# Optimization experiments

Measured on AMD Instinct MI355X. Metric: run time of the kernel, lower is better.

Reference implementation:

```python
import jax, jax.numpy as jnp
import numpy as np

EPS = 1e-5

def _conv3x3(x, w, b):
    # standard 3x3 conv, stride 1, padding 1, NCHW/OIHW
    y = jax.lax.conv_general_dilated(x, w, window_strides=(1, 1), padding=((1, 1), (1, 1)),
                                     dimension_numbers=('NCHW', 'OIHW', 'NCHW'))
    return y + b[None, :, None, None]

def _deform_sample(x, offset):
    # x: [B,C,H,W], offset: [B,2*9,H,W] (per kernel point: (dy,dx), torchvision layout)
    # returns bilinear-sampled im2col columns [B,C,9,H,W] with zero padding outside
    B, C, H, W = x.shape
    off = offset.reshape(B, 9, 2, H, W)
    off_y, off_x = off[:, :, 0], off[:, :, 1]                      # [B,9,H,W]
    k = jnp.arange(9)
    ky = (k // 3 - 1).astype(x.dtype)                               # kernel dy in {-1,0,1}
    kx = (k % 3 - 1).astype(x.dtype)                                # kernel dx in {-1,0,1}
    py = jnp.arange(H, dtype=x.dtype)[None, None, :, None] + ky[None, :, None, None] + off_y
    px = jnp.arange(W, dtype=x.dtype)[None, None, None, :] + kx[None, :, None, None] + off_x
    y0 = jnp.floor(py)
    x0 = jnp.floor(px)
    xf = x.reshape(B, C, H * W)
    acc = jnp.zeros((B, C, 9, H, W), x.dtype)
    for dy in (0.0, 1.0):
        for dx in (0.0, 1.0):
            iy = y0 + dy
            ix = x0 + dx
            wgt = (1.0 - jnp.abs(py - iy)) * (1.0 - jnp.abs(px - ix))
            valid = (iy >= 0) & (iy <= H - 1) & (ix >= 0) & (ix <= W - 1)
            wgt = jnp.where(valid, wgt, 0.0)
            idx = jnp.clip(iy, 0, H - 1).astype(jnp.int32) * W + jnp.clip(ix, 0, W - 1).astype(jnp.int32)
            g = jax.vmap(lambda xb, ib: jnp.take(xb, ib, axis=1))(xf, idx.reshape(B, -1))
            acc = acc + wgt[:, None] * g.reshape(B, C, 9, H, W)
    return acc

def setup_inputs() -> dict:
    key = jax.random.key(0)
    ks = jax.random.split(key, 9)
    B, C, O, H, W = 8, 64, 64, 160, 160
    x = jax.random.normal(ks[0], (B, C, H, W), jnp.float32)
    w_off = jax.random.normal(ks[1], (18, C, 3, 3), jnp.float32) * 0.01
    b_off = jax.random.normal(ks[2], (18,), jnp.float32) * 0.01
    w_dcn = jax.random.normal(ks[3], (O, C, 3, 3), jnp.float32) / np.sqrt(C * 9)
    b_dcn = jax.random.normal(ks[4], (O,), jnp.float32) * 0.01
    gamma = 1.0 + 0.1 * jax.random.normal(ks[5], (O,), jnp.float32)
    beta = 0.1 * jax.random.normal(ks[6], (O,), jnp.float32)
    run_mean = 0.1 * jax.random.normal(ks[7], (O,), jnp.float32)
    run_var = 0.5 + jax.random.uniform(ks[8], (O,), jnp.float32)
    return {"x": x, "w_off": w_off, "b_off": b_off, "w_dcn": w_dcn, "b_dcn": b_dcn,
            "gamma": gamma, "beta": beta, "run_mean": run_mean, "run_var": run_var}

def reference(x, w_off, b_off, w_dcn, b_dcn, gamma, beta, run_mean, run_var):
    offset = _conv3x3(x, w_off, b_off)                  # [B,18,H,W]
    cols = _deform_sample(x, offset)                    # [B,C,9,H,W]
    O = w_dcn.shape[0]
    z = jnp.einsum('bckhw,ock->bohw', cols, w_dcn.reshape(O, -1, 9)) + b_dcn[None, :, None, None]
    inv = gamma / jnp.sqrt(run_var + EPS)               # eval-mode BatchNorm
    y = z * inv[None, :, None, None] + (beta - run_mean * inv)[None, :, None, None]
    return jax.nn.relu(y)
```

## Files before the change

kernel.cpp:

```cpp
#include <hip/hip_runtime.h>

#define Hh 160
#define Ww 160
#define HW 25600
#define Bb 8
#define Cc 64
#define Oo 64
#define NPIX (Bb * HW)

#define TROWS 8
#define TCOLS 36
#define TPIX (TROWS * TCOLS)

typedef __bf16 bf16x8 __attribute__((ext_vector_type(8)));
typedef float  f32x4  __attribute__((ext_vector_type(4)));
typedef float  f32x2  __attribute__((ext_vector_type(2)));

__device__ inline unsigned rnd_bf(float a) {
    unsigned u = __float_as_uint(a);
    return (u + 0x7FFFu + ((u >> 16) & 1u)) >> 16;
}
__device__ inline unsigned pack_bf2(float a, float b) {
    unsigned ua = __float_as_uint(a) + 0x8000u;
    unsigned ub = __float_as_uint(b) + 0x8000u;
    return __builtin_amdgcn_perm(ub, ua, 0x07060302);
}
__device__ inline f32x2 up2(unsigned u) {
    f32x2 r;
    r.x = __uint_as_float(u << 16);
    r.y = __uint_as_float(u & 0xffff0000u);
    return r;
}
__device__ inline unsigned blend4(unsigned u00, unsigned u01, unsigned u10, unsigned u11,
                                  float w00, float w01, float w10, float w11) {
    f32x2 r = up2(u00) * w00 + up2(u01) * w01 + up2(u10) * w10 + up2(u11) * w11;
    return pack_bf2(r.x, r.y);
}
union UV { uint4 u; bf16x8 v; };
__device__ inline bf16x8 as_bf(uint4 u) { UV c; c.u = u; return c.v; }

__global__ __launch_bounds__(256) void prep_kernel(
    const float* __restrict__ w_dcn, const float* __restrict__ b_dcn,
    const float* __restrict__ w_off,
    const float* __restrict__ gamma, const float* __restrict__ beta,
    const float* __restrict__ run_mean, const float* __restrict__ run_var,
    unsigned short* __restrict__ wtbf, unsigned short* __restrict__ wofbf,
    float* __restrict__ scaleb)
{
    int i = blockIdx.x * 256 + threadIdx.x;
    if (i < 9 * 8 * 64 * 8) {
        int j = i & 7, l = (i >> 3) & 63, f = (i >> 9) & 7, k = i >> 12;
        int o  = ((f >> 1) << 4) | (l & 15);
        int cc = ((l >> 4) << 3) + ((f & 1) << 5) + j;
        wtbf[i] = (unsigned short)rnd_bf(w_dcn[(o * Cc + cc) * 9 + k]);
    }
    if (i < 9 * 4 * 64 * 8) {
        int j = i & 7, l = (i >> 3) & 63, f = (i >> 9) & 3, k = i >> 11;
        int o  = ((f >> 1) << 4) | (l & 15);
        int cc = ((l >> 4) << 3) + ((f & 1) << 5) + j;
        float v = (o < 18) ? w_off[(o * Cc + cc) * 9 + k] : 0.0f;
        wofbf[i] = (unsigned short)rnd_bf(v);
    }
    if (i < Oo) {
        float inv = gamma[i] * rsqrtf(run_var[i] + 1e-5f);
        scaleb[i]      = inv;
        scaleb[Oo + i] = b_dcn[i] * inv + (beta[i] - run_mean[i] * inv);
    }
}

__global__ __launch_bounds__(256, 4) void xpose_kernel(
    const float* __restrict__ x, unsigned short* __restrict__ xhwc)
{
    __shared__ float tile[64 * 65];
    int blk = blockIdx.x;
    int nb  = (blk & 7) * 400 + (blk >> 3);
    int b = nb / 400, hw0 = (nb % 400) * 64;
    int t = threadIdx.x;
    int lane = t & 63, grp = t >> 6;

    const float* xp = x + (size_t)b * Cc * HW + hw0 + lane;
#pragma unroll
    for (int i = 0; i < 16; ++i) {
        int c = i * 4 + grp;
        tile[lane * 65 + c] = xp[(size_t)c * HW];
    }
    __syncthreads();

    int px  = t >> 2;
    int ch0 = (t & 3) * 16;
    const float* row = tile + px * 65 + ch0;
    unsigned u[8];
#pragma unroll
    for (int j = 0; j < 8; ++j) u[j] = pack_bf2(row[2 * j], row[2 * j + 1]);
    unsigned short* dst = xhwc + ((size_t)(b * HW + hw0 + px)) * 64 + ch0;
    *(uint4*)dst       = make_uint4(u[0], u[1], u[2], u[3]);
    *(uint4*)(dst + 8) = make_uint4(u[4], u[5], u[6], u[7]);
}

#define TRD(PIX, LO, HI) do {                                                  \
    int _pp = (PIX);                                                           \
    int _s  = _pp & 7;                                                         \
    const char* _tb = (const char*)tile + _pp * 128;                           \
    LO = *(const uint4*)(_tb + ((quad ^ _s) << 4));                            \
    HI = *(const uint4*)(_tb + (((quad + 4) ^ _s) << 4));                      \
} while (0)

__global__ __launch_bounds__(512, 6) void dcn_kernel(
    const unsigned short* __restrict__ xhwc,
    const unsigned short* __restrict__ wtbf,
    const unsigned short* __restrict__ wofbf,
    const float* __restrict__ b_off,
    const float* __restrict__ scaleb,
    float* __restrict__ out)
{
    __shared__ __align__(16) unsigned short tile[TPIX * 64];
    __shared__ __align__(16) float offb[128 * 20];

    const int t = threadIdx.x;
    const int lane = t & 63, wv = t >> 6;
    const int m = lane & 15, quad = lane >> 4;

    int blk = blockIdx.x;
    int b   = blk & 7;
    int nb  = blk >> 3;
    int h0  = (nb / 5) * 4;
    int w0  = (nb % 5) * 32;

    const int rloc  = wv >> 1;
    const int chalf = (wv & 1) * 16;
    const int h = h0 + rloc;
    const int w = w0 + chalf + m;
    const int pl_base = rloc * 32 + chalf;

    const unsigned short* xb = xhwc + (size_t)b * HW * 64;
    const unsigned short* xq = xb + quad * 8;

    for (int id = t; id < TPIX * 8; id += 512) {
        int chunk = id & 7, pix = id >> 3;
        int r = pix / TCOLS, c = pix - r * TCOLS;
        int yr = min(max(h0 - 2 + r, 0), Hh - 1);
        int xc = min(max(w0 - 2 + c, 0), Ww - 1);
        uint4 v = *((const uint4*)(xb + ((size_t)yr * Ww + xc) * 64) + chunk);
        *(uint4*)((char*)tile + pix * 128 + ((chunk ^ (pix & 7)) << 4)) = v;
    }
    __syncthreads();

    f32x4 oa0 = {0,0,0,0}, oa1 = {0,0,0,0};
#pragma unroll
    for (int k = 0; k < 9; ++k) {
        int hp = h + k / 3 - 1, wp = w + (k % 3) - 1;
        bool ok = (hp >= 0) & (hp < Hh) & (wp >= 0) & (wp < Ww);
        int r = min(max(hp, 0), Hh - 1) - h0 + 2;
        int c = min(max(wp, 0), Ww - 1) - w0 + 2;
        uint4 r0, r1;
        TRD(r * TCOLS + c, r0, r1);
        if (!ok) { r0 = make_uint4(0,0,0,0); r1 = make_uint4(0,0,0,0); }
        bf16x8 a0 = as_bf(r0), a1 = as_bf(r1);

        const unsigned short* wf = wofbf + (size_t)(k * 4) * 512 + lane * 8;
        bf16x8 b00 = *(const bf16x8*)(wf);
        bf16x8 b01 = *(const bf16x8*)(wf + 512);
        bf16x8 b10 = *(const bf16x8*)(wf + 1024);
        bf16x8 b11 = *(const bf16x8*)(wf + 1536);
        oa0 = __builtin_amdgcn_mfma_f32_16x16x32_bf16(a0, b00, oa0, 0, 0, 0);
        oa0 = __builtin_amdgcn_mfma_f32_16x16x32_bf16(a1, b01, oa0, 0, 0, 0);
        oa1 = __builtin_amdgcn_mfma_f32_16x16x32_bf16(a0, b10, oa1, 0, 0, 0);
        oa1 = __builtin_amdgcn_mfma_f32_16x16x32_bf16(a1, b11, oa1, 0, 0, 0);
    }

    {
        float bo0 = b_off[m];
        float bo1 = (m < 2) ? b_off[16 + m] : 0.0f;
#pragma unroll
        for (int r = 0; r < 4; ++r) {
            int pp = pl_base + quad * 4 + r;
            offb[pp * 20 + m] = oa0[r] + bo0;
            if (m < 2) offb[pp * 20 + 16 + m] = oa1[r] + bo1;
        }
    }
    float oy[9], ox[9];
    {
        const int p20 = (pl_base + m) * 20;
#pragma unroll
        for (int k = 0; k < 9; ++k) {
            f32x2 o = *(const f32x2*)&offb[p20 + 2 * k];
            oy[k] = o.x; ox[k] = o.y;
        }
    }

    f32x4 c0 = {0,0,0,0}, c1 = {0,0,0,0}, c2 = {0,0,0,0}, c3 = {0,0,0,0};
#pragma unroll
    for (int k = 0; k < 9; ++k) {
        float py = (float)(h + k / 3 - 1) + oy[k];
        float px = (float)(w + k % 3 - 1) + ox[k];
        float y0f = floorf(py), x0f = floorf(px);
        float fy = py - y0f, fx = px - x0f;
        int y0 = (int)y0f, x0i = (int)x0f;
        int y1 = y0 + 1, x1 = x0i + 1;
        bool vy0 = (y0 >= 0) & (y0 < Hh), vy1 = (y1 >= 0) & (y1 < Hh);
        bool vx0 = (x0i >= 0) & (x0i < Ww), vx1 = (x1 >= 0) & (x1 < Ww);
        float w00 = (vy0 & vx0) ? (1.0f - fy) * (1.0f - fx) : 0.0f;
        float w01 = (vy0 & vx1) ? (1.0f - fy) * fx : 0.0f;
        float w10 = (vy1 & vx0) ? fy * (1.0f - fx) : 0.0f;
        float w11 = (vy1 & vx1) ? fy * fx : 0.0f;
        int cy0 = min(max(y0, 0), Hh - 1), cy1 = min(max(y1, 0), Hh - 1);
        int cx0 = min(max(x0i, 0), Ww - 1), cx1 = min(max(x1, 0), Ww - 1);

        int r0 = cy0 - h0 + 2, r1 = cy1 - h0 + 2;
        int d0 = cx0 - w0 + 2, d1 = cx1 - w0 + 2;
        int inw = ((unsigned)r0 <= 7u) & ((unsigned)r1 <= 7u) &
                  ((unsigned)d0 <= 35u) & ((unsigned)d1 <= 35u);

        uint4 a00, h00, a01, h01, a10, h10, a11, h11;
        if (__all(inw)) {
            TRD(r0 * TCOLS + d0, a00, h00);
            TRD(r0 * TCOLS + d1, a01, h01);
            TRD(r1 * TCOLS + d0, a10, h10);
            TRD(r1 * TCOLS + d1, a11, h11);
        } else {
            const unsigned short* s00 = xq + (size_t)(cy0 * Ww + cx0) * 64;
            const unsigned short* s01 = xq + (size_t)(cy0 * Ww + cx1) * 64;
            const unsigned short* s10 = xq + (size_t)(cy1 * Ww + cx0) * 64;
            const unsigned short* s11 = xq + (size_t)(cy1 * Ww + cx1) * 64;
            a00 = *(const uint4*)(s00); h00 = *(const uint4*)(s00 + 32);
            a01 = *(const uint4*)(s01); h01 = *(const uint4*)(s01 + 32);
            a10 = *(const uint4*)(s10); h10 = *(const uint4*)(s10 + 32);
            a11 = *(const uint4*)(s11); h11 = *(const uint4*)(s11 + 32);
        }

        uint4 o0, o1;
        o0.x = blend4(a00.x, a01.x, a10.x, a11.x, w00, w01, w10, w11);
        o0.y = blend4(a00.y, a01.y, a10.y, a11.y, w00, w01, w10, w11);
        o0.z = blend4(a00.z, a01.z, a10.z, a11.z, w00, w01, w10, w11);
        o0.w = blend4(a00.w, a01.w, a10.w, a11.w, w00, w01, w10, w11);
        o1.x = blend4(h00.x, h01.x, h10.x, h11.x, w00, w01, w10, w11);
        o1.y = blend4(h00.y, h01.y, h10.y, h11.y, w00, w01, w10, w11);
        o1.z = blend4(h00.z, h01.z, h10.z, h11.z, w00, w01, w10, w11);
        o1.w = blend4(h00.w, h01.w, h10.w, h11.w, w00, w01, w10, w11);
        bf16x8 A0 = as_bf(o0), A1 = as_bf(o1);

        const unsigned short* wf = wtbf + (size_t)(k * 8) * 512 + lane * 8;
        bf16x8 B0, B1;
        B0 = *(const bf16x8*)(wf);
        B1 = *(const bf16x8*)(wf + 512);
        c0 = __builtin_amdgcn_mfma_f32_16x16x32_bf16(A0, B0, c0, 0, 0, 0);
        c0 = __builtin_amdgcn_mfma_f32_16x16x32_bf16(A1, B1, c0, 0, 0, 0);
        B0 = *(const bf16x8*)(wf + 1024);
        B1 = *(const bf16x8*)(wf + 1536);
        c1 = __builtin_amdgcn_mfma_f32_16x16x32_bf16(A0, B0, c1, 0, 0, 0);
        c1 = __builtin_amdgcn_mfma_f32_16x16x32_bf16(A1, B1, c1, 0, 0, 0);
        B0 = *(const bf16x8*)(wf + 2048);
        B1 = *(const bf16x8*)(wf + 2560);
        c2 = __builtin_amdgcn_mfma_f32_16x16x32_bf16(A0, B0, c2, 0, 0, 0);
        c2 = __builtin_amdgcn_mfma_f32_16x16x32_bf16(A1, B1, c2, 0, 0, 0);
        B0 = *(const bf16x8*)(wf + 3072);
        B1 = *(const bf16x8*)(wf + 3584);
        c3 = __builtin_amdgcn_mfma_f32_16x16x32_bf16(A0, B0, c3, 0, 0, 0);
        c3 = __builtin_amdgcn_mfma_f32_16x16x32_bf16(A1, B1, c3, 0, 0, 0);
    }

#pragma unroll
    for (int nt = 0; nt < 4; ++nt) {
        f32x4 a = (nt == 0) ? c0 : (nt == 1) ? c1 : (nt == 2) ? c2 : c3;
        int o = nt * 16 + m;
        float sc = scaleb[o];
        float bs = scaleb[Oo + o];
        float4 r;
        r.x = fmaxf(a[0] * sc + bs, 0.0f);
        r.y = fmaxf(a[1] * sc + bs, 0.0f);
        r.z = fmaxf(a[2] * sc + bs, 0.0f);
        r.w = fmaxf(a[3] * sc + bs, 0.0f);
        float* op = out + ((size_t)b * Oo + o) * HW + h * Ww + w0 + chalf + quad * 4;
        *(float4*)op = r;
    }
}

extern "C" void kernel_launch(void* const* d_in, const int* in_sizes, int n_in,
                              void* d_out, int out_size, void* d_ws, size_t ws_size,
                              hipStream_t stream) {
    const float* x        = (const float*)d_in[0];
    const float* w_off    = (const float*)d_in[1];
    const float* b_off    = (const float*)d_in[2];
    const float* w_dcn    = (const float*)d_in[3];
    const float* b_dcn    = (const float*)d_in[4];
    const float* gamma    = (const float*)d_in[5];
    const float* beta     = (const float*)d_in[6];
    const float* run_mean = (const float*)d_in[7];
    const float* run_var  = (const float*)d_in[8];
    float* out = (float*)d_out;

    unsigned short* xhwc  = (unsigned short*)d_ws;
    unsigned short* wtbf  = xhwc + (size_t)NPIX * 64;
    unsigned short* wofbf = wtbf + 9 * 8 * 64 * 8;
    float* scaleb         = (float*)(wofbf + 9 * 4 * 64 * 8);

    prep_kernel<<<(9 * 8 * 64 * 8 + 255) / 256, 256, 0, stream>>>(
        w_dcn, b_dcn, w_off, gamma, beta, run_mean, run_var, wtbf, wofbf, scaleb);

    xpose_kernel<<<NPIX / 64, 256, 0, stream>>>(x, xhwc);

    dcn_kernel<<<NPIX / 128, 512, 0, stream>>>(xhwc, wtbf, wofbf, b_off, scaleb, out);
}
```

Measured before the change: 230.1 us.

## Fuse NCHW-to-bf16 transpose into DCN kernel and stage output through LDS

```diff
diff --git a/kernel.cpp b/kernel.cpp
--- a/kernel.cpp
+++ b/kernel.cpp
@@ -68,35 +68,6 @@
     }
 }
 
-__global__ __launch_bounds__(256, 4) void xpose_kernel(
-    const float* __restrict__ x, unsigned short* __restrict__ xhwc)
-{
-    __shared__ float tile[64 * 65];
-    int blk = blockIdx.x;
-    int nb  = (blk & 7) * 400 + (blk >> 3);
-    int b = nb / 400, hw0 = (nb % 400) * 64;
-    int t = threadIdx.x;
-    int lane = t & 63, grp = t >> 6;
-
-    const float* xp = x + (size_t)b * Cc * HW + hw0 + lane;
-#pragma unroll
-    for (int i = 0; i < 16; ++i) {
-        int c = i * 4 + grp;
-        tile[lane * 65 + c] = xp[(size_t)c * HW];
-    }
-    __syncthreads();
-
-    int px  = t >> 2;
-    int ch0 = (t & 3) * 16;
-    const float* row = tile + px * 65 + ch0;
-    unsigned u[8];
-#pragma unroll
-    for (int j = 0; j < 8; ++j) u[j] = pack_bf2(row[2 * j], row[2 * j + 1]);
-    unsigned short* dst = xhwc + ((size_t)(b * HW + hw0 + px)) * 64 + ch0;
-    *(uint4*)dst       = make_uint4(u[0], u[1], u[2], u[3]);
-    *(uint4*)(dst + 8) = make_uint4(u[4], u[5], u[6], u[7]);
-}
-
 #define TRD(PIX, LO, HI) do {                                                  \
     int _pp = (PIX);                                                           \
     int _s  = _pp & 7;                                                         \
@@ -105,8 +76,21 @@
     HI = *(const uint4*)(_tb + (((quad + 4) ^ _s) << 4));                      \
 } while (0)
 
+#define GATHF(CY, CX, A, H) do {                                               \
+    const float* _sp = xbf + (size_t)(quad * 8) * HW + ((CY) * Ww + (CX));     \
+    A = make_uint4(pack_bf2(_sp[0],      _sp[HW]),                             \
+                   pack_bf2(_sp[2 * HW], _sp[3 * HW]),                         \
+                   pack_bf2(_sp[4 * HW], _sp[5 * HW]),                         \
+                   pack_bf2(_sp[6 * HW], _sp[7 * HW]));                        \
+    const float* _hp = _sp + (size_t)32 * HW;                                  \
+    H = make_uint4(pack_bf2(_hp[0],      _hp[HW]),                             \
+                   pack_bf2(_hp[2 * HW], _hp[3 * HW]),                         \
+                   pack_bf2(_hp[4 * HW], _hp[5 * HW]),                         \
+                   pack_bf2(_hp[6 * HW], _hp[7 * HW]));                        \
+} while (0)
+
 __global__ __launch_bounds__(512, 6) void dcn_kernel(
-    const unsigned short* __restrict__ xhwc,
+    const float* __restrict__ x,
     const unsigned short* __restrict__ wtbf,
     const unsigned short* __restrict__ wofbf,
     const float* __restrict__ b_off,
@@ -132,16 +116,22 @@
     const int w = w0 + chalf + m;
     const int pl_base = rloc * 32 + chalf;
 
-    const unsigned short* xb = xhwc + (size_t)b * HW * 64;
-    const unsigned short* xq = xb + quad * 8;
-
-    for (int id = t; id < TPIX * 8; id += 512) {
-        int chunk = id & 7, pix = id >> 3;
-        int r = pix / TCOLS, c = pix - r * TCOLS;
+    const float* xbf = x + (size_t)b * Cc * HW;
+
+#pragma unroll
+    for (int it = 0; it < 18; ++it) {
+        int id  = t + it * 512;
+        int col = id % 36;
+        int rr  = id / 36;
+        int r   = rr & 7;
+        int c2  = rr >> 3;
         int yr = min(max(h0 - 2 + r, 0), Hh - 1);
-        int xc = min(max(w0 - 2 + c, 0), Ww - 1);
-        uint4 v = *((const uint4*)(xb + ((size_t)yr * Ww + xc) * 64) + chunk);
-        *(uint4*)((char*)tile + pix * 128 + ((chunk ^ (pix & 7)) << 4)) = v;
+        int xc = min(max(w0 - 2 + col, 0), Ww - 1);
+        const float* sp = xbf + (size_t)(c2 * 2) * HW + (yr * Ww + xc);
+        unsigned v = pack_bf2(sp[0], sp[HW]);
+        int pix = r * TCOLS + col;
+        *(unsigned*)((char*)tile + pix * 128
+                     + ((((c2 >> 2) ^ (pix & 7)) << 4) + ((c2 & 3) << 2))) = v;
     }
     __syncthreads();
 
@@ -218,14 +208,10 @@
             TRD(r1 * TCOLS + d0, a10, h10);
             TRD(r1 * TCOLS + d1, a11, h11);
         } else {
-            const unsigned short* s00 = xq + (size_t)(cy0 * Ww + cx0) * 64;
-            const unsigned short* s01 = xq + (size_t)(cy0 * Ww + cx1) * 64;
-            const unsigned short* s10 = xq + (size_t)(cy1 * Ww + cx0) * 64;
-            const unsigned short* s11 = xq + (size_t)(cy1 * Ww + cx1) * 64;
-            a00 = *(const uint4*)(s00); h00 = *(const uint4*)(s00 + 32);
-            a01 = *(const uint4*)(s01); h01 = *(const uint4*)(s01 + 32);
-            a10 = *(const uint4*)(s10); h10 = *(const uint4*)(s10 + 32);
-            a11 = *(const uint4*)(s11); h11 = *(const uint4*)(s11 + 32);
+            GATHF(cy0, cx0, a00, h00);
+            GATHF(cy0, cx1, a01, h01);
+            GATHF(cy1, cx0, a10, h10);
+            GATHF(cy1, cx1, a11, h11);
         }
 
         uint4 o0, o1;
@@ -259,19 +245,35 @@
         c3 = __builtin_amdgcn_mfma_f32_16x16x32_bf16(A1, B1, c3, 0, 0, 0);
     }
 
+    __syncthreads();
+    float* obuf = (float*)tile;
 #pragma unroll
     for (int nt = 0; nt < 4; ++nt) {
         f32x4 a = (nt == 0) ? c0 : (nt == 1) ? c1 : (nt == 2) ? c2 : c3;
         int o = nt * 16 + m;
         float sc = scaleb[o];
         float bs = scaleb[Oo + o];
-        float4 r;
-        r.x = fmaxf(a[0] * sc + bs, 0.0f);
-        r.y = fmaxf(a[1] * sc + bs, 0.0f);
-        r.z = fmaxf(a[2] * sc + bs, 0.0f);
-        r.w = fmaxf(a[3] * sc + bs, 0.0f);
-        float* op = out + ((size_t)b * Oo + o) * HW + h * Ww + w0 + chalf + quad * 4;
-        *(float4*)op = r;
+        f32x4 r;
+        r[0] = fmaxf(a[0] * sc + bs, 0.0f);
+        r[1] = fmaxf(a[1] * sc + bs, 0.0f);
+        r[2] = fmaxf(a[2] * sc + bs, 0.0f);
+        r[3] = fmaxf(a[3] * sc + bs, 0.0f);
+        *(f32x4*)&obuf[o * 132 + pl_base + quad * 4] = r;
+    }
+    __syncthreads();
+    {
+        int o = t >> 3, part = t & 7;
+        const float* src = obuf + o * 132 + part * 16;
+        float* dst = out + ((size_t)b * Oo + o) * HW
+                   + (h0 + (part >> 1)) * Ww + w0 + (part & 1) * 16;
+        float4 v0 = *(const float4*)(src);
+        float4 v1 = *(const float4*)(src + 4);
+        float4 v2 = *(const float4*)(src + 8);
+        float4 v3 = *(const float4*)(src + 12);
+        *(float4*)(dst)      = v0;
+        *(float4*)(dst + 4)  = v1;
+        *(float4*)(dst + 8)  = v2;
+        *(float4*)(dst + 12) = v3;
     }
 }
 
@@ -289,15 +291,12 @@
     const float* run_var  = (const float*)d_in[8];
     float* out = (float*)d_out;
 
-    unsigned short* xhwc  = (unsigned short*)d_ws;
-    unsigned short* wtbf  = xhwc + (size_t)NPIX * 64;
+    unsigned short* wtbf  = (unsigned short*)d_ws;
     unsigned short* wofbf = wtbf + 9 * 8 * 64 * 8;
     float* scaleb         = (float*)(wofbf + 9 * 4 * 64 * 8);
 
     prep_kernel<<<(9 * 8 * 64 * 8 + 255) / 256, 256, 0, stream>>>(
         w_dcn, b_dcn, w_off, gamma, beta, run_mean, run_var, wtbf, wofbf, scaleb);
 
-    xpose_kernel<<<NPIX / 64, 256, 0, stream>>>(x, xhwc);
-
-    dcn_kernel<<<NPIX / 128, 512, 0, stream>>>(xhwc, wtbf, wofbf, b_off, scaleb, out);
-}
+    dcn_kernel<<<NPIX / 128, 512, 0, stream>>>(x, wtbf, wofbf, b_off, scaleb, out);
+}
```

New measurement: 209.7 us. -8.9%, faster.
